# Kernel tuning notes

Hardware: AMD Instinct MI355X
Metric: run time of the kernel (lower is better)

## Reference

```python
import jax, jax.numpy as jnp
import numpy as np

NUM_HEADS = 16
NUM_GROUPS = 32  # min(C//4, 32) with C=1024
EPS = 1e-6       # flax GroupNorm default


def setup_inputs() -> dict:
    key = jax.random.key(0)
    ks = jax.random.split(key, 3)
    B, L, C = 2, 2048, 1024
    x = jax.random.normal(ks[0], (B, L, C), dtype=jnp.float32)
    gn_scale = jnp.ones((C,), jnp.float32)
    gn_bias = jnp.zeros((C,), jnp.float32)
    qkv_w = jax.random.normal(ks[1], (C, 3 * C), jnp.float32) * (C ** -0.5)
    qkv_b = jnp.zeros((3 * C,), jnp.float32)
    proj_w = jax.random.normal(ks[2], (C, C), jnp.float32) * 1e-5  # default_init(1e-10) ~ tiny
    proj_b = jnp.zeros((C,), jnp.float32)
    return {"x": x, "gn_scale": gn_scale, "gn_bias": gn_bias,
            "qkv_w": qkv_w, "qkv_b": qkv_b, "proj_w": proj_w, "proj_b": proj_b}


def reference(x, gn_scale, gn_bias, qkv_w, qkv_b, proj_w, proj_b):
    B, L, C = x.shape
    H = NUM_HEADS
    hd = C // H
    # GroupNorm over (L, channels-in-group)
    xg = x.reshape(B, L, NUM_GROUPS, C // NUM_GROUPS)
    mu = jnp.mean(xg, axis=(1, 3), keepdims=True)
    var = jnp.var(xg, axis=(1, 3), keepdims=True)
    xn = ((xg - mu) * jax.lax.rsqrt(var + EPS)).reshape(B, L, C)
    xn = xn * gn_scale + gn_bias
    # 1x1-conv QKV projection == dense
    qkv = xn @ qkv_w + qkv_b                       # [B, L, 3C]
    qkv = qkv.reshape(B, L, H, 3 * hd)             # interleaved per-head q|k|v
    q, k, v = jnp.split(qkv, 3, axis=-1)           # each [B, L, H, hd]
    scale = 1.0 / jnp.sqrt(hd)
    logits = jnp.einsum('btnh,bfnh->bnft', k, q * scale)  # [B, H, L, L]
    weights = jax.nn.softmax(logits, axis=-1)
    h = jnp.einsum('bnft,btnh->bfnh', weights, v).reshape(B, L, C)
    h = h @ proj_w + proj_b
    # CombineResidualSkip, project_skip=False
    return (x + h) / np.sqrt(2.0)
```

## Files before the change

### kernel.cpp

```cpp
#include <hip/hip_runtime.h>
#include <hip/hip_bf16.h>

typedef __hip_bfloat16 bf16;
typedef __attribute__((ext_vector_type(8))) __bf16 bf16x8;
typedef __attribute__((ext_vector_type(4))) float floatx4;

#define NB 2
#define NL 2048
#define NC 1024
#define NH 16
#define ND 64

__device__ __forceinline__ void async_copy16(void* lds, const void* g) {
  __builtin_amdgcn_global_load_lds(
      (__attribute__((address_space(1))) void*)(const_cast<void*>(g)),
      (__attribute__((address_space(3))) void*)(lds), 16, 0, 0);
}

__device__ __forceinline__ floatx4 mfma16(bf16x8 a, bf16x8 b, floatx4 c) {
  return __builtin_amdgcn_mfma_f32_16x16x32_bf16(a, b, c, 0, 0, 0);
}

__global__ __launch_bounds__(256) void gn_part_kernel(
    const float* __restrict__ x, float2* __restrict__ part) {
  int bg = blockIdx.x >> 3, sl = blockIdx.x & 7;
  int b = bg >> 5, g = bg & 31;
  const float* base = x + (size_t)b * NL * NC + (size_t)(sl * 256) * NC + g * 32;
  float s = 0.f, ss = 0.f;
  for (int vi = threadIdx.x; vi < 2048; vi += 256) {
    int l = vi >> 3, j = (vi & 7) * 4;
    float4 u = *(const float4*)(base + (size_t)l * NC + j);
    s += u.x + u.y + u.z + u.w;
    ss += u.x * u.x + u.y * u.y + u.z * u.z + u.w * u.w;
  }
  for (int off = 32; off; off >>= 1) {
    s += __shfl_down(s, off);
    ss += __shfl_down(ss, off);
  }
  __shared__ float rs[4], rss[4];
  int wave = threadIdx.x >> 6, lane = threadIdx.x & 63;
  if (lane == 0) { rs[wave] = s; rss[wave] = ss; }
  __syncthreads();
  if (threadIdx.x == 0) {
    part[blockIdx.x] = make_float2(rs[0] + rs[1] + rs[2] + rs[3],
                                   rss[0] + rss[1] + rss[2] + rss[3]);
  }
}

__global__ __launch_bounds__(256) void gn_apply_kernel(
    const float* __restrict__ x, const float2* __restrict__ part,
    const float* __restrict__ scale, const float* __restrict__ bias,
    bf16* __restrict__ xn) {
  size_t idx = (size_t)blockIdx.x * 256 + threadIdx.x;
  size_t e = idx * 8;
  int c = (int)(e & (NC - 1));
  int b = (int)(e >> 21);
  int bg = b * 32 + (c >> 5);
  float s = 0.f, ss = 0.f;
#pragma unroll
  for (int i = 0; i < 8; ++i) {
    float2 p = part[bg * 8 + i];
    s += p.x; ss += p.y;
  }
  float mean = s * (1.f / 65536.f);
  float var = ss * (1.f / 65536.f) - mean * mean;
  float rstd = rsqrtf(var + 1e-6f);
  float4 x0 = *(const float4*)(x + e);
  float4 x1 = *(const float4*)(x + e + 4);
  float4 s0 = *(const float4*)(scale + c);
  float4 s1 = *(const float4*)(scale + c + 4);
  float4 b0 = *(const float4*)(bias + c);
  float4 b1 = *(const float4*)(bias + c + 4);
  float xv[8] = {x0.x, x0.y, x0.z, x0.w, x1.x, x1.y, x1.z, x1.w};
  float sv[8] = {s0.x, s0.y, s0.z, s0.w, s1.x, s1.y, s1.z, s1.w};
  float bv[8] = {b0.x, b0.y, b0.z, b0.w, b1.x, b1.y, b1.z, b1.w};
  bf16 o[8];
#pragma unroll
  for (int k = 0; k < 8; ++k)
    o[k] = __float2bfloat16((xv[k] - mean) * rstd * sv[k] + bv[k]);
  *(uint4*)(xn + e) = *(const uint4*)o;
}

__global__ void transpose_f32_bf16(const float* __restrict__ in,
                                   bf16* __restrict__ out, int R, int C) {
  __shared__ float t[32][33];
  int c0 = blockIdx.x * 32, r0 = blockIdx.y * 32;
#pragma unroll
  for (int j = 0; j < 4; ++j)
    t[threadIdx.y + j * 8][threadIdx.x] =
        in[(size_t)(r0 + threadIdx.y + j * 8) * C + c0 + threadIdx.x];
  __syncthreads();
#pragma unroll
  for (int j = 0; j < 4; ++j)
    out[(size_t)(c0 + threadIdx.y + j * 8) * R + r0 + threadIdx.x] =
        __float2bfloat16(t[threadIdx.x][threadIdx.y + j * 8]);
}

template <int MODE>
__global__ __launch_bounds__(256) void gemm_kernel(
    const bf16* __restrict__ A, const bf16* __restrict__ Bt,
    const float* __restrict__ biasv, const float* __restrict__ xres,
    bf16* __restrict__ Qo, bf16* __restrict__ Ko, bf16* __restrict__ Vto,
    float* __restrict__ out, int M, int N, int K) {
  __shared__ bf16 As[128 * 32];
  __shared__ bf16 Bs[128 * 32];
  int tid = threadIdx.x, wave = tid >> 6, lane = tid & 63;
  int col = lane & 15, quad = lane >> 4;
  int mB = blockIdx.y * 128, nB = blockIdx.x * 128;
  int wm = (wave >> 1) * 64, wn = (wave & 1) * 64;
  floatx4 acc[4][4];
#pragma unroll
  for (int i = 0; i < 4; ++i)
#pragma unroll
    for (int j = 0; j < 4; ++j) acc[i][j] = (floatx4){0.f, 0.f, 0.f, 0.f};

  int rowOff = wave * 32 + (lane >> 2);
  int kOff = (lane & 3) * 8;

  for (int k0 = 0; k0 < K; k0 += 32) {
    __syncthreads();
    const bf16* ga = A + (size_t)(mB + rowOff) * K + k0 + kOff;
    async_copy16(&As[(wave * 32) * 32], ga);
    async_copy16(&As[(wave * 32 + 16) * 32], ga + (size_t)16 * K);
    const bf16* gb = Bt + (size_t)(nB + rowOff) * K + k0 + kOff;
    async_copy16(&Bs[(wave * 32) * 32], gb);
    async_copy16(&Bs[(wave * 32 + 16) * 32], gb + (size_t)16 * K);
    __syncthreads();
    bf16x8 af[4], bfr[4];
#pragma unroll
    for (int mi = 0; mi < 4; ++mi)
      af[mi] = *(const bf16x8*)&As[(wm + mi * 16 + col) * 32 + quad * 8];
#pragma unroll
    for (int ni = 0; ni < 4; ++ni)
      bfr[ni] = *(const bf16x8*)&Bs[(wn + ni * 16 + col) * 32 + quad * 8];
#pragma unroll
    for (int mi = 0; mi < 4; ++mi)
#pragma unroll
      for (int ni = 0; ni < 4; ++ni)
        acc[mi][ni] = mfma16(af[mi], bfr[ni], acc[mi][ni]);
  }

#pragma unroll
  for (int mi = 0; mi < 4; ++mi)
#pragma unroll
    for (int ni = 0; ni < 4; ++ni)
#pragma unroll
      for (int r = 0; r < 4; ++r) {
        int row = mB + wm + mi * 16 + quad * 4 + r;
        int ncol = nB + wn + ni * 16 + col;
        float v = acc[mi][ni][r] + biasv[ncol];
        if (MODE == 0) {
          int b = row >> 11, f = row & 2047;
          int h = ncol / 192, rr = ncol - h * 192;
          size_t bhl = ((size_t)(b * NH + h) * NL + f);
          if (rr < 64)
            Qo[bhl * 64 + rr] = __float2bfloat16(v * 0.125f);
          else if (rr < 128)
            Ko[bhl * 64 + rr - 64] = __float2bfloat16(v);
          else
            Vto[((size_t)(b * NH + h) * 64 + (rr - 128)) * NL + f] = __float2bfloat16(v);
        } else {
          size_t o = (size_t)row * N + ncol;
          out[o] = (xres[o] + v) * 0.70710678118654752f;
        }
      }
}

__global__ __launch_bounds__(256, 2) void attn_kernel(
    const bf16* __restrict__ Q, const bf16* __restrict__ Kb,
    const bf16* __restrict__ Vt, bf16* __restrict__ hout) {
  int qt = blockIdx.x, bh = blockIdx.y;
  int b = bh >> 4, h = bh & 15;
  int tid = threadIdx.x, wave = tid >> 6, lane = tid & 63;
  int m = lane & 15, quad = lane >> 4;

  __shared__ bf16 Kd[2][4096];
  __shared__ bf16 Vd[2][4096];
  __shared__ bf16 QPs[4][2304];

  bf16* Qw = QPs[wave];
  bf16* Psw = QPs[wave];

  const bf16* Kg = Kb + (size_t)bh * NL * 64;
  const bf16* Vg = Vt + (size_t)bh * 64 * NL;

  {
    const bf16* Qg = Q + ((size_t)bh * NL + qt * 128 + wave * 32) * 64;
#pragma unroll
    for (int i = 0; i < 4; ++i) {
      int slot = i * 64 + lane;
      int r = slot >> 3, sc = slot & 7;
      int cg = sc ^ (r & 7);
      *(uint4*)&Qw[r * 64 + sc * 8] = *(const uint4*)&Qg[(size_t)r * 64 + cg * 8];
    }
  }
  bf16x8 bq[2][2];
#pragma unroll
  for (int nf = 0; nf < 2; ++nf)
#pragma unroll
    for (int c = 0; c < 2; ++c)
      bq[nf][c] = *(const bf16x8*)
          &Qw[(nf * 16 + m) * 64 + ((c * 4 + quad) ^ (m & 7)) * 8];

  float lrow[2] = {0.f, 0.f};
  floatx4 o[2][4];
#pragma unroll
  for (int nf = 0; nf < 2; ++nf)
#pragma unroll
    for (int di = 0; di < 4; ++di) o[nf][di] = (floatx4){0.f, 0.f, 0.f, 0.f};

  int srow = lane >> 3, schunk = lane & 7;

  auto stage = [&](int bufi, int t0) {
#pragma unroll
    for (int i = 0; i < 2; ++i) {
      int r0 = wave * 16 + i * 8;
      int r = r0 + srow;
      int cg = schunk ^ (r & 7);
      async_copy16(&Kd[bufi][r0 * 64], Kg + (size_t)(t0 + r) * 64 + cg * 8);
      async_copy16(&Vd[bufi][r0 * 64], Vg + (size_t)r * NL + t0 + cg * 8);
    }
  };

  stage(0, 0);
  __syncthreads();

  int buf = 0;
  for (int t0 = 0; t0 < NL; t0 += 64) {
    if (t0 + 64 < NL) stage(buf ^ 1, t0 + 64);

    const bf16* Kbase = Kd[buf];
    const bf16* Vbase = Vd[buf];

    floatx4 s[2][4];
#pragma unroll
    for (int nf = 0; nf < 2; ++nf)
#pragma unroll
      for (int ti = 0; ti < 4; ++ti) s[nf][ti] = (floatx4){0.f, 0.f, 0.f, 0.f};
#pragma unroll
    for (int ti = 0; ti < 4; ++ti)
#pragma unroll
      for (int c = 0; c < 2; ++c) {
        bf16x8 ak = *(const bf16x8*)
            &Kbase[(ti * 16 + m) * 64 + ((c * 4 + quad) ^ (m & 7)) * 8];
        s[0][ti] = mfma16(ak, bq[0][c], s[0][ti]);
        s[1][ti] = mfma16(ak, bq[1][c], s[1][ti]);
      }

#pragma unroll
    for (int nf = 0; nf < 2; ++nf) {
      float ls = 0.f;
#pragma unroll
      for (int ti = 0; ti < 4; ++ti)
#pragma unroll
        for (int r = 0; r < 4; ++r) {
          float p = __expf(s[nf][ti][r]);
          s[nf][ti][r] = p;
          ls += p;
        }
      ls += __shfl_xor(ls, 16);
      ls += __shfl_xor(ls, 32);
      lrow[nf] += ls;
#pragma unroll
      for (int ti = 0; ti < 4; ++ti) {
        bf16 pk[4];
#pragma unroll
        for (int r = 0; r < 4; ++r) pk[r] = __float2bfloat16(s[nf][ti][r]);
        *(uint2*)&Psw[(nf * 16 + m) * 72 + ti * 16 + quad * 4] = *(const uint2*)pk;
      }
    }

#pragma unroll
    for (int c = 0; c < 2; ++c) {
      bf16x8 bp[2];
#pragma unroll
      for (int nf = 0; nf < 2; ++nf)
        bp[nf] = *(const bf16x8*)&Psw[(nf * 16 + m) * 72 + c * 32 + quad * 8];
#pragma unroll
      for (int di = 0; di < 4; ++di) {
        bf16x8 av = *(const bf16x8*)
            &Vbase[(di * 16 + m) * 64 + ((c * 4 + quad) ^ (m & 7)) * 8];
        o[0][di] = mfma16(av, bp[0], o[0][di]);
        o[1][di] = mfma16(av, bp[1], o[1][di]);
      }
    }

    __syncthreads();
    buf ^= 1;
  }

#pragma unroll
  for (int nf = 0; nf < 2; ++nf) {
    float rl = 1.f / lrow[nf];
    int l = qt * 128 + wave * 32 + nf * 16 + m;
    bf16* hp = hout + (size_t)(b * NL + l) * NC + h * 64;
#pragma unroll
    for (int di = 0; di < 4; ++di) {
      bf16 pk[4];
#pragma unroll
      for (int r = 0; r < 4; ++r) pk[r] = __float2bfloat16(o[nf][di][r] * rl);
      *(uint2*)&hp[di * 16 + quad * 4] = *(const uint2*)pk;
    }
  }
}

extern "C" void kernel_launch(void* const* d_in, const int* in_sizes, int n_in,
                              void* d_out, int out_size, void* d_ws, size_t ws_size,
                              hipStream_t stream) {
  const float* x = (const float*)d_in[0];
  const float* gn_scale = (const float*)d_in[1];
  const float* gn_bias = (const float*)d_in[2];
  const float* qkv_w = (const float*)d_in[3];
  const float* qkv_b = (const float*)d_in[4];
  const float* proj_w = (const float*)d_in[5];
  const float* proj_b = (const float*)d_in[6];
  float* out = (float*)d_out;

  bf16* xn = (bf16*)d_out;

  char* ws = (char*)d_ws;
  float2* part = (float2*)ws;
  bf16* Qb = (bf16*)(ws + 4096);
  bf16* Kbuf = Qb + 4194304;
  bf16* Vt = Kbuf + 4194304;
  bf16* hat = Vt + 4194304;
  bf16* wqkvT = hat;
  bf16* projT = Qb;

  gn_part_kernel<<<512, 256, 0, stream>>>(x, part);
  gn_apply_kernel<<<2048, 256, 0, stream>>>(x, part, gn_scale, gn_bias, xn);
  transpose_f32_bf16<<<dim3(96, 32), dim3(32, 8), 0, stream>>>(qkv_w, wqkvT, 1024, 3072);
  gemm_kernel<0><<<dim3(24, 32), 256, 0, stream>>>(
      xn, wqkvT, qkv_b, nullptr, Qb, Kbuf, Vt, nullptr, 4096, 3072, 1024);
  attn_kernel<<<dim3(16, 32), 256, 0, stream>>>(Qb, Kbuf, Vt, hat);
  transpose_f32_bf16<<<dim3(32, 32), dim3(32, 8), 0, stream>>>(proj_w, projT, 1024, 1024);
  gemm_kernel<1><<<dim3(8, 32), 256, 0, stream>>>(
      hat, projT, proj_b, x, nullptr, nullptr, nullptr, out, 4096, 1024, 1024);
}
```

Before: 225.6 us.

## Split attention keys across wave pairs and shrink projection GEMM N tile

The attention kernel now processes 64 queries per block: each pair of waves shares the same 32 query rows and splits every 64-key tile in half. Partial outputs and row sums are combined through LDS at the end. This doubles the grid, shrinks the per-wave P buffer and allows 4 blocks per CU, in exchange for a cross-wave reduction and more K/V staging per query. The output projection GEMM is also templated on N tile and launched with 64-wide tiles to double its block count and fill more CUs.

```diff
diff --git a/kernel.cpp b/kernel.cpp
--- a/kernel.cpp
+++ b/kernel.cpp
@@ -96,25 +96,27 @@
         __float2bfloat16(t[threadIdx.x][threadIdx.y + j * 8]);
 }
 
-template <int MODE>
+template <int MODE, int NT>
 __global__ __launch_bounds__(256) void gemm_kernel(
     const bf16* __restrict__ A, const bf16* __restrict__ Bt,
     const float* __restrict__ biasv, const float* __restrict__ xres,
     bf16* __restrict__ Qo, bf16* __restrict__ Ko, bf16* __restrict__ Vto,
     float* __restrict__ out, int M, int N, int K) {
+  constexpr int NFR = NT / 32;
   __shared__ bf16 As[128 * 32];
-  __shared__ bf16 Bs[128 * 32];
+  __shared__ bf16 Bs[NT * 32];
   int tid = threadIdx.x, wave = tid >> 6, lane = tid & 63;
   int col = lane & 15, quad = lane >> 4;
-  int mB = blockIdx.y * 128, nB = blockIdx.x * 128;
-  int wm = (wave >> 1) * 64, wn = (wave & 1) * 64;
-  floatx4 acc[4][4];
+  int mB = blockIdx.y * 128, nB = blockIdx.x * NT;
+  int wm = (wave >> 1) * 64, wn = (wave & 1) * (NT / 2);
+  floatx4 acc[4][NFR];
 #pragma unroll
   for (int i = 0; i < 4; ++i)
 #pragma unroll
-    for (int j = 0; j < 4; ++j) acc[i][j] = (floatx4){0.f, 0.f, 0.f, 0.f};
+    for (int j = 0; j < NFR; ++j) acc[i][j] = (floatx4){0.f, 0.f, 0.f, 0.f};
 
   int rowOff = wave * 32 + (lane >> 2);
+  int rowOffB = (NT == 128) ? rowOff : (wave * 16 + (lane >> 2));
   int kOff = (lane & 3) * 8;
 
   for (int k0 = 0; k0 < K; k0 += 32) {
@@ -122,28 +124,32 @@
     const bf16* ga = A + (size_t)(mB + rowOff) * K + k0 + kOff;
     async_copy16(&As[(wave * 32) * 32], ga);
     async_copy16(&As[(wave * 32 + 16) * 32], ga + (size_t)16 * K);
-    const bf16* gb = Bt + (size_t)(nB + rowOff) * K + k0 + kOff;
-    async_copy16(&Bs[(wave * 32) * 32], gb);
-    async_copy16(&Bs[(wave * 32 + 16) * 32], gb + (size_t)16 * K);
+    const bf16* gb = Bt + (size_t)(nB + rowOffB) * K + k0 + kOff;
+    if (NT == 128) {
+      async_copy16(&Bs[(wave * 32) * 32], gb);
+      async_copy16(&Bs[(wave * 32 + 16) * 32], gb + (size_t)16 * K);
+    } else {
+      async_copy16(&Bs[(wave * 16) * 32], gb);
+    }
     __syncthreads();
-    bf16x8 af[4], bfr[4];
+    bf16x8 af[4], bfr[NFR];
 #pragma unroll
     for (int mi = 0; mi < 4; ++mi)
       af[mi] = *(const bf16x8*)&As[(wm + mi * 16 + col) * 32 + quad * 8];
 #pragma unroll
-    for (int ni = 0; ni < 4; ++ni)
+    for (int ni = 0; ni < NFR; ++ni)
       bfr[ni] = *(const bf16x8*)&Bs[(wn + ni * 16 + col) * 32 + quad * 8];
 #pragma unroll
     for (int mi = 0; mi < 4; ++mi)
 #pragma unroll
-      for (int ni = 0; ni < 4; ++ni)
+      for (int ni = 0; ni < NFR; ++ni)
         acc[mi][ni] = mfma16(af[mi], bfr[ni], acc[mi][ni]);
   }
 
 #pragma unroll
   for (int mi = 0; mi < 4; ++mi)
 #pragma unroll
-    for (int ni = 0; ni < 4; ++ni)
+    for (int ni = 0; ni < NFR; ++ni)
 #pragma unroll
       for (int r = 0; r < 4; ++r) {
         int row = mB + wm + mi * 16 + quad * 4 + r;
@@ -166,41 +172,33 @@
       }
 }
 
-__global__ __launch_bounds__(256, 2) void attn_kernel(
+__global__ __launch_bounds__(256, 4) void attn_kernel(
     const bf16* __restrict__ Q, const bf16* __restrict__ Kb,
     const bf16* __restrict__ Vt, bf16* __restrict__ hout) {
   int qt = blockIdx.x, bh = blockIdx.y;
   int b = bh >> 4, h = bh & 15;
   int tid = threadIdx.x, wave = tid >> 6, lane = tid & 63;
   int m = lane & 15, quad = lane >> 4;
+  int tg = wave >> 1, th = wave & 1;
 
   __shared__ bf16 Kd[2][4096];
   __shared__ bf16 Vd[2][4096];
-  __shared__ bf16 QPs[4][2304];
-
-  bf16* Qw = QPs[wave];
-  bf16* Psw = QPs[wave];
+  __shared__ bf16 Pp[4][1024];
+
+  bf16* Psw = Pp[wave];
 
   const bf16* Kg = Kb + (size_t)bh * NL * 64;
   const bf16* Vg = Vt + (size_t)bh * 64 * NL;
 
+  bf16x8 bq[2][2];
   {
-    const bf16* Qg = Q + ((size_t)bh * NL + qt * 128 + wave * 32) * 64;
-#pragma unroll
-    for (int i = 0; i < 4; ++i) {
-      int slot = i * 64 + lane;
-      int r = slot >> 3, sc = slot & 7;
-      int cg = sc ^ (r & 7);
-      *(uint4*)&Qw[r * 64 + sc * 8] = *(const uint4*)&Qg[(size_t)r * 64 + cg * 8];
-    }
-  }
-  bf16x8 bq[2][2];
-#pragma unroll
-  for (int nf = 0; nf < 2; ++nf)
-#pragma unroll
-    for (int c = 0; c < 2; ++c)
-      bq[nf][c] = *(const bf16x8*)
-          &Qw[(nf * 16 + m) * 64 + ((c * 4 + quad) ^ (m & 7)) * 8];
+    const bf16* Qg = Q + ((size_t)bh * NL + qt * 64 + tg * 32) * 64;
+#pragma unroll
+    for (int nf = 0; nf < 2; ++nf)
+#pragma unroll
+      for (int c = 0; c < 2; ++c)
+        bq[nf][c] = *(const bf16x8*)&Qg[(size_t)(nf * 16 + m) * 64 + c * 32 + quad * 8];
+  }
 
   float lrow[2] = {0.f, 0.f};
   floatx4 o[2][4];
@@ -232,17 +230,17 @@
     const bf16* Kbase = Kd[buf];
     const bf16* Vbase = Vd[buf];
 
-    floatx4 s[2][4];
+    floatx4 s[2][2];
 #pragma unroll
     for (int nf = 0; nf < 2; ++nf)
 #pragma unroll
-      for (int ti = 0; ti < 4; ++ti) s[nf][ti] = (floatx4){0.f, 0.f, 0.f, 0.f};
-#pragma unroll
-    for (int ti = 0; ti < 4; ++ti)
+      for (int ti = 0; ti < 2; ++ti) s[nf][ti] = (floatx4){0.f, 0.f, 0.f, 0.f};
+#pragma unroll
+    for (int ti = 0; ti < 2; ++ti)
 #pragma unroll
       for (int c = 0; c < 2; ++c) {
         bf16x8 ak = *(const bf16x8*)
-            &Kbase[(ti * 16 + m) * 64 + ((c * 4 + quad) ^ (m & 7)) * 8];
+            &Kbase[(th * 32 + ti * 16 + m) * 64 + ((c * 4 + quad) ^ (m & 7)) * 8];
         s[0][ti] = mfma16(ak, bq[0][c], s[0][ti]);
         s[1][ti] = mfma16(ak, bq[1][c], s[1][ti]);
       }
@@ -251,7 +249,7 @@
     for (int nf = 0; nf < 2; ++nf) {
       float ls = 0.f;
 #pragma unroll
-      for (int ti = 0; ti < 4; ++ti)
+      for (int ti = 0; ti < 2; ++ti)
 #pragma unroll
         for (int r = 0; r < 4; ++r) {
           float p = __expf(s[nf][ti][r]);
@@ -262,44 +260,68 @@
       ls += __shfl_xor(ls, 32);
       lrow[nf] += ls;
 #pragma unroll
-      for (int ti = 0; ti < 4; ++ti) {
+      for (int ti = 0; ti < 2; ++ti) {
         bf16 pk[4];
 #pragma unroll
         for (int r = 0; r < 4; ++r) pk[r] = __float2bfloat16(s[nf][ti][r]);
-        *(uint2*)&Psw[(nf * 16 + m) * 72 + ti * 16 + quad * 4] = *(const uint2*)pk;
+        int ct = ti * 2 + (quad >> 1);
+        *(uint2*)&Psw[(nf * 16 + m) * 32 + ((ct ^ (m & 3)) * 8) + (quad & 1) * 4] =
+            *(const uint2*)pk;
       }
     }
 
-#pragma unroll
-    for (int c = 0; c < 2; ++c) {
-      bf16x8 bp[2];
-#pragma unroll
-      for (int nf = 0; nf < 2; ++nf)
-        bp[nf] = *(const bf16x8*)&Psw[(nf * 16 + m) * 72 + c * 32 + quad * 8];
-#pragma unroll
-      for (int di = 0; di < 4; ++di) {
-        bf16x8 av = *(const bf16x8*)
-            &Vbase[(di * 16 + m) * 64 + ((c * 4 + quad) ^ (m & 7)) * 8];
-        o[0][di] = mfma16(av, bp[0], o[0][di]);
-        o[1][di] = mfma16(av, bp[1], o[1][di]);
-      }
+    bf16x8 bp[2];
+#pragma unroll
+    for (int nf = 0; nf < 2; ++nf)
+      bp[nf] = *(const bf16x8*)&Psw[(nf * 16 + m) * 32 + ((quad ^ (m & 3)) * 8)];
+#pragma unroll
+    for (int di = 0; di < 4; ++di) {
+      bf16x8 av = *(const bf16x8*)
+          &Vbase[(di * 16 + m) * 64 + ((th * 4 + quad) ^ (m & 7)) * 8];
+      o[0][di] = mfma16(av, bp[0], o[0][di]);
+      o[1][di] = mfma16(av, bp[1], o[1][di]);
     }
 
     __syncthreads();
     buf ^= 1;
   }
 
-#pragma unroll
-  for (int nf = 0; nf < 2; ++nf) {
-    float rl = 1.f / lrow[nf];
-    int l = qt * 128 + wave * 32 + nf * 16 + m;
-    bf16* hp = hout + (size_t)(b * NL + l) * NC + h * 64;
-#pragma unroll
-    for (int di = 0; di < 4; ++di) {
-      bf16 pk[4];
-#pragma unroll
-      for (int r = 0; r < 4; ++r) pk[r] = __float2bfloat16(o[nf][di][r] * rl);
-      *(uint2*)&hp[di * 16 + quad * 4] = *(const uint2*)pk;
+  float* So = (float*)Kd;
+  float* Sl = (float*)Vd;
+  if (th == 1) {
+#pragma unroll
+    for (int nf = 0; nf < 2; ++nf) {
+      Sl[tg * 128 + nf * 64 + lane] = lrow[nf];
+#pragma unroll
+      for (int di = 0; di < 4; ++di)
+#pragma unroll
+        for (int r = 0; r < 4; ++r)
+          So[tg * 2048 + (nf * 16 + di * 4 + r) * 64 + lane] = o[nf][di][r];
+    }
+  }
+  __syncthreads();
+  if (th == 0) {
+#pragma unroll
+    for (int nf = 0; nf < 2; ++nf) {
+      lrow[nf] += Sl[tg * 128 + nf * 64 + lane];
+#pragma unroll
+      for (int di = 0; di < 4; ++di)
+#pragma unroll
+        for (int r = 0; r < 4; ++r)
+          o[nf][di][r] += So[tg * 2048 + (nf * 16 + di * 4 + r) * 64 + lane];
+    }
+#pragma unroll
+    for (int nf = 0; nf < 2; ++nf) {
+      float rl = 1.f / lrow[nf];
+      int l = qt * 64 + tg * 32 + nf * 16 + m;
+      bf16* hp = hout + (size_t)(b * NL + l) * NC + h * 64;
+#pragma unroll
+      for (int di = 0; di < 4; ++di) {
+        bf16 pk[4];
+#pragma unroll
+        for (int r = 0; r < 4; ++r) pk[r] = __float2bfloat16(o[nf][di][r] * rl);
+        *(uint2*)&hp[di * 16 + quad * 4] = *(const uint2*)pk;
+      }
     }
   }
 }
@@ -330,10 +352,10 @@
   gn_part_kernel<<<512, 256, 0, stream>>>(x, part);
   gn_apply_kernel<<<2048, 256, 0, stream>>>(x, part, gn_scale, gn_bias, xn);
   transpose_f32_bf16<<<dim3(96, 32), dim3(32, 8), 0, stream>>>(qkv_w, wqkvT, 1024, 3072);
-  gemm_kernel<0><<<dim3(24, 32), 256, 0, stream>>>(
+  gemm_kernel<0, 128><<<dim3(24, 32), 256, 0, stream>>>(
       xn, wqkvT, qkv_b, nullptr, Qb, Kbuf, Vt, nullptr, 4096, 3072, 1024);
-  attn_kernel<<<dim3(16, 32), 256, 0, stream>>>(Qb, Kbuf, Vt, hat);
+  attn_kernel<<<dim3(32, 32), 256, 0, stream>>>(Qb, Kbuf, Vt, hat);
   transpose_f32_bf16<<<dim3(32, 32), dim3(32, 8), 0, stream>>>(proj_w, projT, 1024, 1024);
-  gemm_kernel<1><<<dim3(8, 32), 256, 0, stream>>>(
+  gemm_kernel<1, 64><<<dim3(16, 32), 256, 0, stream>>>(
       hat, projT, proj_b, x, nullptr, nullptr, nullptr, out, 4096, 1024, 1024);
 }
```

Result: no change. 227.4 us (+0.8%).
